# Kernel optimization log

Measured on AMD Instinct MI355X. Metric: run time of the kernel, lower is better.

Reference implementation:

```python
import jax, jax.numpy as jnp
import numpy as np

N, E, B, A = 102400, 1638400, 256, 7


def setup_inputs() -> dict:
    key = jax.random.key(0)
    ks = jax.random.split(key, 24)
    rn = lambda k, s, sc=0.1: jax.random.normal(k, s, jnp.float32) * sc
    return {
        "x": jax.random.normal(ks[0], (N, 5), jnp.float32),
        "edge_index": jax.random.randint(ks[1], (2, E), 0, N, jnp.int32),
        "edge_attr": jax.random.normal(ks[2], (E, 1), jnp.float32),
        "agent_state": jax.random.normal(ks[3], (B, 34), jnp.float32),
        "pool_batch": jnp.sort(jax.random.randint(ks[4], (N,), 0, B, jnp.int32)),
        # GATConv params (heads=1, concat): lin [5,64], lin_edge [1,64], att vectors [64], bias [64]
        "W_gat": rn(ks[5], (5, 64)), "att_src": rn(ks[6], (64,)), "att_dst": rn(ks[7], (64,)),
        "W_edge": rn(ks[8], (1, 64)), "att_edge": rn(ks[9], (64,)), "b_gat": rn(ks[10], (64,)),
        "W_fc1": rn(ks[11], (64, 128)), "b_fc1": rn(ks[12], (128,)),
        "W_fc2": rn(ks[13], (34, 64)), "b_fc2": rn(ks[14], (64,)),
        "W_v1": rn(ks[15], (192, 128)), "b_v1": rn(ks[16], (128,)),
        "W_v2": rn(ks[17], (128, 1)), "b_v2": rn(ks[18], (1,)),
        "W_a1": rn(ks[19], (192, 128)), "b_a1": rn(ks[20], (128,)),
        "W_a2": rn(ks[21], (128, A)), "b_a2": rn(ks[22], (A,)),
    }


def _gat(x, edge_index, edge_attr, W_gat, att_src, att_dst, W_edge, att_edge, b_gat):
    n = x.shape[0]
    # add self-loops (PyG default), self-loop edge_attr = mean of edge_attr
    loop = jnp.arange(n, dtype=edge_index.dtype)
    src = jnp.concatenate([edge_index[0], loop])
    dst = jnp.concatenate([edge_index[1], loop])
    ea = jnp.concatenate([edge_attr, jnp.broadcast_to(edge_attr.mean(0), (n, edge_attr.shape[1]))], 0)
    h = x @ W_gat                                  # [N,64]
    a_s = h @ att_src                              # [N]
    a_d = h @ att_dst                              # [N]
    a_e = (ea @ W_edge) @ att_edge                 # [E+N]
    alpha = jax.nn.leaky_relu(a_s[src] + a_d[dst] + a_e, 0.2)
    # segment softmax over incoming edges per destination node
    m = jax.ops.segment_max(alpha, dst, num_segments=n)
    ex = jnp.exp(alpha - m[dst])
    s = jax.ops.segment_sum(ex, dst, num_segments=n)
    w = ex / (s[dst] + 1e-16)
    out = jax.ops.segment_sum(w[:, None] * h[src], dst, num_segments=n)
    return out + b_gat


def reference(x, edge_index, edge_attr, agent_state, pool_batch,
              W_gat, att_src, att_dst, W_edge, att_edge, b_gat,
              W_fc1, b_fc1, W_fc2, b_fc2,
              W_v1, b_v1, W_v2, b_v2, W_a1, b_a1, W_a2, b_a2):
    h = _gat(x, edge_index, edge_attr, W_gat, att_src, att_dst, W_edge, att_edge, b_gat)
    h = jax.nn.relu(h @ W_fc1 + b_fc1)             # [N,128]
    # global mean pool over graphs
    ssum = jax.ops.segment_sum(h, pool_batch, num_segments=B)
    cnt = jax.ops.segment_sum(jnp.ones((h.shape[0],), h.dtype), pool_batch, num_segments=B)
    g = ssum / jnp.maximum(cnt, 1.0)[:, None]      # [B,128]
    a = jax.nn.relu(agent_state @ W_fc2 + b_fc2)   # [B,64]
    z = jnp.concatenate([g, a], -1)                # [B,192]
    value = jax.nn.relu(z @ W_v1 + b_v1) @ W_v2 + b_v2
    adv = jax.nn.relu(z @ W_a1 + b_a1) @ W_a2 + b_a2
    return value + adv - adv.mean(-1, keepdims=True)
```

## Files before the change

kernel.cpp:

```cpp
#include <hip/hip_runtime.h>
#include <hip/hip_fp16.h>
#include <math.h>

#define NPB   512
#define NPBL  9
#define HSTR  5
#define MAXR  256
#define TILE  2048
#define RPT   8
#define GCS   16
#define SLICES 8

static __device__ __forceinline__ float lrelu(float x) { return x > 0.0f ? x : 0.2f * x; }

static __device__ __forceinline__ unsigned pk2(float a, float b) {
    __half2 h = __floats2half2_rn(a, b);
    return *reinterpret_cast<unsigned*>(&h);
}
static __device__ __forceinline__ float2 up2(unsigned u) {
    __half2 h = *reinterpret_cast<__half2*>(&u);
    return __half22float2(h);
}


__global__ void k_setup(const float* __restrict__ W_gat, const float* __restrict__ att_src,
                        const float* __restrict__ att_dst, const float* __restrict__ W_edge,
                        const float* __restrict__ att_edge, const float* __restrict__ b_gat,
                        const float* __restrict__ W_fc1, const float* __restrict__ b_fc1,
                        float* __restrict__ consts, unsigned* __restrict__ gcur,
                        float* __restrict__ epart8) {
    int t = threadIdx.x;
    for (int i = t; i < MAXR * GCS; i += 128) gcur[i] = 0u;
    if (t < 8) epart8[t] = 0.f;
    if (t == 0) {
        float c = 0.f;
        for (int k = 0; k < 64; k++) c += W_edge[k] * att_edge[k];
        consts[1] = c;
    }
    if (t < 5) {
        float a = 0.f, b = 0.f;
        for (int c = 0; c < 64; c++) {
            float w = W_gat[t * 64 + c];
            a += w * att_src[c];
            b += w * att_dst[c];
        }
        consts[2 + t] = a;
        consts[7 + t] = b;
    }
    float bcv = b_fc1[t];
    for (int c = 0; c < 64; c++) bcv += b_gat[c] * W_fc1[c * 128 + t];
    consts[16 + t] = bcv;
    for (int k = 0; k < 5; k++) {
        float w = 0.f;
        for (int c = 0; c < 64; c++) w += W_gat[k * 64 + c] * W_fc1[c * 128 + t];
        consts[144 + k * 128 + t] = w;
    }
}

__global__ void k_np1(const float* __restrict__ x, const float* __restrict__ consts,
                      uint4* __restrict__ xh, float* __restrict__ a_s, float* __restrict__ a_d,
                      const int* __restrict__ pb, int* __restrict__ bstart,
                      const int* __restrict__ src, const int* __restrict__ dst,
                      const float* __restrict__ ea,
                      uint2* __restrict__ slab, unsigned* __restrict__ gcur,
                      float* __restrict__ epart8,
                      int N, int B, int E, int R, int CAP, int nbl) {
    if ((int)blockIdx.x < nbl) {
        int i = blockIdx.x * blockDim.x + threadIdx.x;
        if (i >= N) return;
        const float* xi = x + (size_t)i * 5;
        float x0 = xi[0], x1 = xi[1], x2 = xi[2], x3 = xi[3], x4 = xi[4];
        float as = x0 * consts[2] + x1 * consts[3] + x2 * consts[4] + x3 * consts[5] + x4 * consts[6];
        float ad = x0 * consts[7] + x1 * consts[8] + x2 * consts[9] + x3 * consts[10] + x4 * consts[11];
        uint4 pkv;
        pkv.x = pk2(x0, x1);
        pkv.y = pk2(x2, x3);
        pkv.z = pk2(x4, 1.0f);
        pkv.w = __float_as_uint(as);
        xh[i] = pkv;
        a_s[i] = as;
        a_d[i] = ad;
        int cur = pb[i];
        int prev = (i == 0) ? -1 : pb[i - 1];
        for (int b = prev + 1; b <= cur; b++) bstart[b] = i;
        if (i == N - 1)
            for (int b = cur + 1; b <= B; b++) bstart[b] = N;
        return;
    }
    __shared__ unsigned hist[MAXR], lbase[MAXR], gbase[MAXR], scan[256];
    __shared__ uint2 staged[TILE];
    __shared__ unsigned char bof[TILE];
    __shared__ float esum[256];
    int t = threadIdx.x;
    int e0 = ((int)blockIdx.x - nbl) * TILE;
    int n = E - e0; if (n > TILE) n = TILE;
    for (int i = t; i < MAXR; i += 256) hist[i] = 0;
    __syncthreads();
    unsigned key[RPT]; float val[RPT]; unsigned brk[RPT];
    float ce = consts[1];
    float easc = 0.f;
#pragma unroll
    for (int k = 0; k < RPT; k++) {
        int idx = t + k * 256;
        brk[k] = 0xFFFFFFFFu;
        if (idx < n) {
            int e = e0 + idx;
            int d = dst[e];
            unsigned b = (unsigned)d >> NPBL;
            key[k] = ((unsigned)src[e] << NPBL) | ((unsigned)d & (NPB - 1));
            float eav = ea[e];
            easc += eav;
            val[k] = ce * eav;
            unsigned r = atomicAdd(&hist[b], 1u);
            brk[k] = (b << 12) | r;
        }
    }
    __syncthreads();
    unsigned v = (t < R) ? hist[t] : 0;
    if (t < R) gbase[t] = atomicAdd(&gcur[t * GCS], v);
    scan[t] = v;
    __syncthreads();
    for (int off = 1; off < 256; off <<= 1) {
        unsigned add = (t >= off) ? scan[t - off] : 0;
        __syncthreads();
        scan[t] += add;
        __syncthreads();
    }
    if (t < R) lbase[t] = scan[t] - v;
    __syncthreads();
#pragma unroll
    for (int k = 0; k < RPT; k++) {
        if (brk[k] != 0xFFFFFFFFu) {
            unsigned b = brk[k] >> 12, r = brk[k] & 4095u;
            unsigned pos = lbase[b] + r;
            staged[pos] = make_uint2(key[k], __float_as_uint(val[k]));
            bof[pos] = (unsigned char)b;
        }
    }
    __syncthreads();
    for (int i = t; i < n; i += 256) {
        unsigned b = bof[i];
        unsigned slot = gbase[b] + (unsigned)i - lbase[b];
        if (slot < (unsigned)CAP) slab[(size_t)b * CAP + slot] = staged[i];
    }
    esum[t] = easc;
    __syncthreads();
    for (int o = 128; o > 0; o >>= 1) {
        if (t < o) esum[t] += esum[t + o];
        __syncthreads();
    }
    if (t == 0) unsafeAtomicAdd(&epart8[blockIdx.x & 7], esum[0]);
}

__global__ void k_p2(const uint2* __restrict__ slab, const unsigned* __restrict__ gcur,
                     const uint4* __restrict__ xh, const float* __restrict__ a_d,
                     unsigned* __restrict__ partials, const float* __restrict__ epart8,
                     float* __restrict__ consts_w, int S, int CAP, int N) {
    __shared__ __half2 accH[NPB * HSTR];
    __shared__ float adl[NPB];
    int t = threadIdx.x;
    int s = blockIdx.x, r = blockIdx.y;
    if (s == 0 && r == 0 && t == 0) {
        float se = 0.f;
        for (int i = 0; i < 8; i++) se += epart8[i];
        consts_w[0] = se;
    }
    for (int i = t; i < NPB; i += 256) {
        int node = r * NPB + i;
        adl[i] = (node < N) ? a_d[node] : 0.f;
    }
    __half2 z2 = __floats2half2_rn(0.f, 0.f);
    for (int i = t; i < NPB * HSTR; i += 256) accH[i] = z2;
    __syncthreads();
    unsigned cnt = gcur[r * GCS]; if (cnt > (unsigned)CAP) cnt = CAP;
    unsigned L = (cnt + (unsigned)S - 1) / (unsigned)S;
    unsigned i0 = (unsigned)s * L, i1 = i0 + L; if (i1 > cnt) i1 = cnt;
    const uint2* sl = slab + (size_t)r * CAP;
    for (unsigned i = i0 + t; i < i1; i += 256) {
        uint2 rec = sl[i];
        uint4 v = xh[rec.x >> NPBL];
        unsigned dl = rec.x & (NPB - 1);
        float al = __uint_as_float(v.w) + adl[dl] + __uint_as_float(rec.y);
        float ex = __expf(lrelu(al));
        __half2 ex2 = __half2half2(__float2half(ex));
        __half2* a = accH + dl * HSTR;
        unsafeAtomicAdd(a + 0, __hmul2(ex2, *reinterpret_cast<const __half2*>(&v.x)));
        unsafeAtomicAdd(a + 1, __hmul2(ex2, *reinterpret_cast<const __half2*>(&v.y)));
        unsafeAtomicAdd(a + 2, __hmul2(ex2, *reinterpret_cast<const __half2*>(&v.z)));
    }
    __syncthreads();
    unsigned* out = partials + (size_t)(r * S + s) * (NPB * 3);
    for (int j = t; j < NPB * 3; j += 256) {
        int comp = j >> NPBL, dl = j & (NPB - 1);
        out[j] = *reinterpret_cast<unsigned*>(&accH[dl * HSTR + comp]);
    }
}

__global__ void k_p3(const unsigned* __restrict__ partials, const float* __restrict__ x,
                     const float* __restrict__ a_s, const float* __restrict__ a_d,
                     const float* __restrict__ consts, float* __restrict__ y,
                     int N, int S, float inv_E) {
    int i = blockIdx.x * blockDim.x + threadIdx.x;
    if (i >= N) return;
    int r = i >> NPBL, dl = i & (NPB - 1);
    float2 y01 = make_float2(0.f, 0.f), y23 = make_float2(0.f, 0.f), y4s = make_float2(0.f, 0.f);
    const unsigned* p = partials + (size_t)r * S * (NPB * 3) + dl;
    for (int s = 0; s < S; s++) {
        const unsigned* q = p + (size_t)s * (NPB * 3);
        float2 a = up2(q[0 * NPB]), b = up2(q[1 * NPB]), c = up2(q[2 * NPB]);
        y01.x += a.x; y01.y += a.y;
        y23.x += b.x; y23.y += b.y;
        y4s.x += c.x; y4s.y += c.y;
    }
    const float* xi = x + (size_t)i * 5;
    float x0 = xi[0], x1 = xi[1], x2 = xi[2], x3 = xi[3], x4 = xi[4];
    float mean_ea = consts[0] * inv_E;
    float aself = lrelu(a_s[i] + a_d[i] + consts[1] * mean_ea);
    float exs = __expf(aself);
    float inv = 1.f / (y4s.y + exs + 1e-16f);
    y[0 * (size_t)N + i] = (y01.x + exs * x0) * inv;
    y[1 * (size_t)N + i] = (y01.y + exs * x1) * inv;
    y[2 * (size_t)N + i] = (y23.x + exs * x2) * inv;
    y[3 * (size_t)N + i] = (y23.y + exs * x3) * inv;
    y[4 * (size_t)N + i] = (y4s.x + exs * x4) * inv;
}

__global__ void k_pool(const float* __restrict__ y, const float* __restrict__ consts,
                       const int* __restrict__ bstart, float* __restrict__ g4, int B, int N) {
    int l = threadIdx.x;
    int b = blockIdx.x >> 2, q = blockIdx.x & 3;
    int st = bstart[b], en = bstart[b + 1];
    int len = en - st;
    int qlen = (len + 3) >> 2;
    int i0 = st + q * qlen;
    int i1 = i0 + qlen;
    if (i0 > en) i0 = en;
    if (i1 > en) i1 = en;
    float w0 = consts[144 + l], w1 = consts[272 + l], w2 = consts[400 + l],
          w3 = consts[528 + l], w4 = consts[656 + l];
    float bc = consts[16 + l];
    const float* y0 = y;
    const float* y1p = y + (size_t)N;
    const float* y2p = y + 2 * (size_t)N;
    const float* y3p = y + 3 * (size_t)N;
    const float* y4p = y + 4 * (size_t)N;
    float a0 = 0.f, a1 = 0.f, a2 = 0.f, a3 = 0.f;
    int i = i0;
    for (; i + 3 < i1; i += 4) {
        float h0 = bc + y0[i] * w0 + y1p[i] * w1 + y2p[i] * w2 + y3p[i] * w3 + y4p[i] * w4;
        float h1 = bc + y0[i+1] * w0 + y1p[i+1] * w1 + y2p[i+1] * w2 + y3p[i+1] * w3 + y4p[i+1] * w4;
        float h2 = bc + y0[i+2] * w0 + y1p[i+2] * w1 + y2p[i+2] * w2 + y3p[i+2] * w3 + y4p[i+2] * w4;
        float h3 = bc + y0[i+3] * w0 + y1p[i+3] * w1 + y2p[i+3] * w2 + y3p[i+3] * w3 + y4p[i+3] * w4;
        a0 += fmaxf(h0, 0.f);
        a1 += fmaxf(h1, 0.f);
        a2 += fmaxf(h2, 0.f);
        a3 += fmaxf(h3, 0.f);
    }
    for (; i < i1; ++i) {
        float h = bc + y0[i] * w0 + y1p[i] * w1 + y2p[i] * w2 + y3p[i] * w3 + y4p[i] * w4;
        a0 += fmaxf(h, 0.f);
    }
    g4[((size_t)q * B + b) * 128 + l] = (a0 + a1) + (a2 + a3);
}

__global__ void k_head(const float* __restrict__ g4, const int* __restrict__ bstart,
                       const float* __restrict__ agent_state, const float* __restrict__ W_fc2,
                       const float* __restrict__ b_fc2, const float* __restrict__ W_v1,
                       const float* __restrict__ b_v1, const float* __restrict__ W_v2,
                       const float* __restrict__ b_v2, const float* __restrict__ W_a1,
                       const float* __restrict__ b_a1, const float* __restrict__ W_a2,
                       const float* __restrict__ b_a2, float* __restrict__ out, int A, int B) {
    __shared__ float z[192];
    __shared__ float v1s[128], a1s[128], red[128];
    __shared__ float advs[8];
    int b = blockIdx.x, t = threadIdx.x;
    float cnt = (float)(bstart[b + 1] - bstart[b]);
    cnt = cnt < 1.f ? 1.f : cnt;
    z[t] = (g4[(size_t)b * 128 + t] + g4[((size_t)B + b) * 128 + t]
          + g4[(2 * (size_t)B + b) * 128 + t] + g4[(3 * (size_t)B + b) * 128 + t]) / cnt;
    if (t < 64) {
        float a = b_fc2[t];
        const float* as_ = agent_state + b * 34;
        for (int k = 0; k < 34; k++) a += as_[k] * W_fc2[k * 64 + t];
        z[128 + t] = fmaxf(a, 0.f);
    }
    __syncthreads();
    float v = b_v1[t], a = b_a1[t];
#pragma unroll 4
    for (int j = 0; j < 192; j++) {
        float zj = z[j];
        v += zj * W_v1[j * 128 + t];
        a += zj * W_a1[j * 128 + t];
    }
    v1s[t] = fmaxf(v, 0.f);
    a1s[t] = fmaxf(a, 0.f);
    __syncthreads();
    red[t] = v1s[t] * W_v2[t];
    __syncthreads();
    for (int o = 64; o > 0; o >>= 1) {
        if (t < o) red[t] += red[t + o];
        __syncthreads();
    }
    float value = red[0] + b_v2[0];
    if (t < A) {
        float ad = b_a2[t];
        for (int j = 0; j < 128; j++) ad += a1s[j] * W_a2[j * A + t];
        advs[t] = ad;
    }
    __syncthreads();
    if (t == 0) {
        float m = 0.f;
        for (int j = 0; j < A; j++) m += advs[j];
        m *= (1.f / (float)A);
        for (int j = 0; j < A; j++) out[b * A + j] = value + advs[j] - m;
    }
}

extern "C" void kernel_launch(void* const* d_in, const int* in_sizes, int n_in,
                              void* d_out, int out_size, void* d_ws, size_t ws_size,
                              hipStream_t stream) {
    const float* x        = (const float*)d_in[0];
    const int* edge_index = (const int*)d_in[1];
    const float* ea       = (const float*)d_in[2];
    const float* agent    = (const float*)d_in[3];
    const int* pool_batch = (const int*)d_in[4];
    const float* W_gat    = (const float*)d_in[5];
    const float* att_src  = (const float*)d_in[6];
    const float* att_dst  = (const float*)d_in[7];
    const float* W_edge   = (const float*)d_in[8];
    const float* att_edge = (const float*)d_in[9];
    const float* b_gat    = (const float*)d_in[10];
    const float* W_fc1    = (const float*)d_in[11];
    const float* b_fc1    = (const float*)d_in[12];
    const float* W_fc2    = (const float*)d_in[13];
    const float* b_fc2    = (const float*)d_in[14];
    const float* W_v1     = (const float*)d_in[15];
    const float* b_v1     = (const float*)d_in[16];
    const float* W_v2     = (const float*)d_in[17];
    const float* b_v2     = (const float*)d_in[18];
    const float* W_a1     = (const float*)d_in[19];
    const float* b_a1     = (const float*)d_in[20];
    const float* W_a2     = (const float*)d_in[21];
    const float* b_a2     = (const float*)d_in[22];

    const int N = in_sizes[0] / 5;
    const int E = in_sizes[2];
    const int B = in_sizes[3] / 34;
    const int A = out_size / B;
    const float inv_E = 1.0f / (float)E;

    const int* src = edge_index;
    const int* dst = edge_index + E;

    const int R = (N + NPB - 1) / NPB;
    int capBase = (E + R - 1) / R;
    const int CAP = capBase + capBase / 16 + 256;

    char* ws = (char*)d_ws;
    size_t off = 0;
    auto take = [&](size_t bytes) {
        size_t o = off;
        off = (off + bytes + 255) & ~(size_t)255;
        return o;
    };
    size_t o_consts = take(4096);
    size_t o_gcur   = take((size_t)MAXR * GCS * 4);
    size_t o_epart8 = take(8 * 4);
    size_t o_xh     = take((size_t)N * 16);
    size_t o_as     = take((size_t)N * 4);
    size_t o_ad     = take((size_t)N * 4);
    size_t o_y      = take((size_t)N * 5 * 4);
    size_t o_bstart = take((size_t)(B + 1) * 4);
    size_t o_g4     = take((size_t)4 * B * 128 * 4);
    size_t o_slab   = take((size_t)R * CAP * 8);
    size_t o_part   = off;
    size_t perS = (size_t)R * NPB * 3 * 4;
    int S = SLICES;
    while (S > 1 && o_part + (size_t)S * perS > ws_size) S--;

    float* consts   = (float*)(ws + o_consts);
    unsigned* gcur  = (unsigned*)(ws + o_gcur);
    float* epart8   = (float*)(ws + o_epart8);
    uint4* xh       = (uint4*)(ws + o_xh);
    float* a_s      = (float*)(ws + o_as);
    float* a_d      = (float*)(ws + o_ad);
    float* y        = (float*)(ws + o_y);
    int* bstart     = (int*)(ws + o_bstart);
    float* g4       = (float*)(ws + o_g4);
    uint2* slab     = (uint2*)(ws + o_slab);
    unsigned* partials = (unsigned*)(ws + o_part);

    k_setup<<<1, 128, 0, stream>>>(W_gat, att_src, att_dst, W_edge, att_edge, b_gat,
                                   W_fc1, b_fc1, consts, gcur, epart8);

    int nbl = (N + 255) / 256;
    int ebl = (E + TILE - 1) / TILE;
    k_np1<<<nbl + ebl, 256, 0, stream>>>(x, consts, xh, a_s, a_d, pool_batch, bstart,
                                         src, dst, ea, slab, gcur, epart8,
                                         N, B, E, R, CAP, nbl);
    dim3 g2grid(S, R);
    k_p2<<<g2grid, 256, 0, stream>>>(slab, gcur, xh, a_d, partials, epart8, consts, S, CAP, N);
    k_p3<<<nbl, 256, 0, stream>>>(partials, x, a_s, a_d, consts, y, N, S, inv_E);
    k_pool<<<4 * B, 128, 0, stream>>>(y, consts, bstart, g4, B, N);
    k_head<<<B, 128, 0, stream>>>(g4, bstart, agent, W_fc2, b_fc2, W_v1, b_v1, W_v2, b_v2,
                                  W_a1, b_a1, W_a2, b_a2, (float*)d_out, A, B);
}
```

Before: 124.2 us.

## Split head MLP across 512 threads with partial sums and wave-reduced advantage

```diff
diff --git a/kernel.cpp b/kernel.cpp
--- a/kernel.cpp
+++ b/kernel.cpp
@@ -271,44 +271,60 @@
                        const float* __restrict__ b_a1, const float* __restrict__ W_a2,
                        const float* __restrict__ b_a2, float* __restrict__ out, int A, int B) {
     __shared__ float z[192];
-    __shared__ float v1s[128], a1s[128], red[128];
+    __shared__ float part[4][128];
+    __shared__ float va[256];
+    __shared__ float red[128];
     __shared__ float advs[8];
     int b = blockIdx.x, t = threadIdx.x;
-    float cnt = (float)(bstart[b + 1] - bstart[b]);
-    cnt = cnt < 1.f ? 1.f : cnt;
-    z[t] = (g4[(size_t)b * 128 + t] + g4[((size_t)B + b) * 128 + t]
-          + g4[(2 * (size_t)B + b) * 128 + t] + g4[(3 * (size_t)B + b) * 128 + t]) / cnt;
-    if (t < 64) {
-        float a = b_fc2[t];
+    int col = t & 127, grp = t >> 7;
+    if (t < 128) {
+        float cnt = (float)(bstart[b + 1] - bstart[b]);
+        cnt = cnt < 1.f ? 1.f : cnt;
+        z[t] = (g4[(size_t)b * 128 + t] + g4[((size_t)B + b) * 128 + t]
+              + g4[(2 * (size_t)B + b) * 128 + t] + g4[(3 * (size_t)B + b) * 128 + t]) / cnt;
+    } else if (t < 192) {
+        int c = t - 128;
+        float a = b_fc2[c];
         const float* as_ = agent_state + b * 34;
-        for (int k = 0; k < 34; k++) a += as_[k] * W_fc2[k * 64 + t];
-        z[128 + t] = fmaxf(a, 0.f);
-    }
-    __syncthreads();
-    float v = b_v1[t], a = b_a1[t];
-#pragma unroll 4
-    for (int j = 0; j < 192; j++) {
-        float zj = z[j];
-        v += zj * W_v1[j * 128 + t];
-        a += zj * W_a1[j * 128 + t];
-    }
-    v1s[t] = fmaxf(v, 0.f);
-    a1s[t] = fmaxf(a, 0.f);
-    __syncthreads();
-    red[t] = v1s[t] * W_v2[t];
+        for (int k = 0; k < 34; k++) a += as_[k] * W_fc2[k * 64 + c];
+        z[128 + c] = fmaxf(a, 0.f);
+    }
+    __syncthreads();
+    {
+        const float* W = (grp & 2) ? W_a1 : W_v1;
+        int j0 = (grp & 1) * 96;
+        float c0 = 0.f, c1 = 0.f, c2 = 0.f, c3 = 0.f;
+        for (int j = j0; j < j0 + 96; j += 4) {
+            c0 += z[j]     * W[(size_t)j * 128 + col];
+            c1 += z[j + 1] * W[(size_t)(j + 1) * 128 + col];
+            c2 += z[j + 2] * W[(size_t)(j + 2) * 128 + col];
+            c3 += z[j + 3] * W[(size_t)(j + 3) * 128 + col];
+        }
+        part[grp][col] = (c0 + c1) + (c2 + c3);
+    }
+    __syncthreads();
+    if (t < 128) {
+        float v = fmaxf(b_v1[t] + part[0][t] + part[1][t], 0.f);
+        va[t] = v;
+        red[t] = v * W_v2[t];
+    } else if (t < 256) {
+        va[t] = fmaxf(b_a1[col] + part[2][col] + part[3][col], 0.f);
+    }
     __syncthreads();
     for (int o = 64; o > 0; o >>= 1) {
         if (t < o) red[t] += red[t + o];
         __syncthreads();
     }
-    float value = red[0] + b_v2[0];
-    if (t < A) {
-        float ad = b_a2[t];
-        for (int j = 0; j < 128; j++) ad += a1s[j] * W_a2[j * A + t];
-        advs[t] = ad;
+    if (t < A * 64) {
+        int oc = t >> 6, lane = t & 63;
+        float s = va[128 + lane] * W_a2[(size_t)lane * A + oc]
+                + va[128 + 64 + lane] * W_a2[(size_t)(64 + lane) * A + oc];
+        for (int o = 32; o > 0; o >>= 1) s += __shfl_down(s, o, 64);
+        if (lane == 0) advs[oc] = s + b_a2[oc];
     }
     __syncthreads();
     if (t == 0) {
+        float value = red[0] + b_v2[0];
         float m = 0.f;
         for (int j = 0; j < A; j++) m += advs[j];
         m *= (1.f / (float)A);
@@ -402,6 +418,6 @@
     k_p2<<<g2grid, 256, 0, stream>>>(slab, gcur, xh, a_d, partials, epart8, consts, S, CAP, N);
     k_p3<<<nbl, 256, 0, stream>>>(partials, x, a_s, a_d, consts, y, N, S, inv_E);
     k_pool<<<4 * B, 128, 0, stream>>>(y, consts, bstart, g4, B, N);
-    k_head<<<B, 128, 0, stream>>>(g4, bstart, agent, W_fc2, b_fc2, W_v1, b_v1, W_v2, b_v2,
+    k_head<<<B, 512, 0, stream>>>(g4, bstart, agent, W_fc2, b_fc2, W_v1, b_v1, W_v2, b_v2,
                                   W_a1, b_a1, W_a2, b_a2, (float*)d_out, A, B);
 }
```

Result: faster. 106.5 us (-14.3%).
